# Kernel optimization log

Hardware: AMD Instinct MI355X
Metric: run time of the kernel (lower is better)

## Reference

```python
import jax, jax.numpy as jnp
import numpy as np

N, E, B = 10000, 160000, 256
IN, DESC = 57, 1217
# (in_dim, heads, out_per_head) for the 4 GATConv layers
CONV_DIMS = [(57, 5, 114), (570, 5, 171), (855, 5, 114), (570, 1, 570)]
FC_DIMS = [(1024 + DESC, 1024), (1024, 2048), (2048, 1024), (1024, 256), (256, 1)]


def setup_inputs() -> dict:
    key = jax.random.key(0)
    cnt = [0]
    def p(shape, scale=0.05):
        cnt[0] += 1
        return jax.random.normal(jax.random.fold_in(key, cnt[0]), shape, jnp.float32) * scale
    d = {}
    d["x"] = jax.random.normal(jax.random.fold_in(key, 100), (N, IN), jnp.float32)
    d["edge_index"] = jax.random.randint(jax.random.fold_in(key, 101), (2, E), 0, N)
    d["batch"] = jnp.sort(jax.random.randint(jax.random.fold_in(key, 102), (N,), 0, B))
    d["desc"] = jax.random.normal(jax.random.fold_in(key, 103), (B, DESC), jnp.float32)
    for i, (ci, H, C) in enumerate(CONV_DIMS, 1):
        d[f"W{i}"] = p((ci, H * C))
        d[f"as{i}"] = p((H, C))
        d[f"ad{i}"] = p((H, C))
        d[f"b{i}"] = jnp.zeros((H * C,), jnp.float32)
    d["Wg"] = p((570, 1024)); d["bg"] = jnp.zeros((1024,), jnp.float32)
    for i, (ci, co) in enumerate(FC_DIMS, 1):
        d[f"Wf{i}"] = p((ci, co))
        d[f"bf{i}"] = jnp.zeros((co,), jnp.float32)
    return d


def gat_conv(x, src, dst, W, a_src, a_dst, b):
    """PyG GATConv (eval mode: attention dropout off), self-loops already in src/dst."""
    n = x.shape[0]
    H, C = a_src.shape
    h = (x @ W).reshape(n, H, C)                      # [N,H,C]
    al_s = (h * a_src).sum(-1)                         # [N,H]
    al_d = (h * a_dst).sum(-1)                         # [N,H]
    e = jax.nn.leaky_relu(al_s[src] + al_d[dst], 0.2)  # [E,H]
    # segment softmax over destination node
    m = jax.ops.segment_max(e, dst, num_segments=n)
    e = jnp.exp(e - m[dst])
    s = jax.ops.segment_sum(e, dst, num_segments=n)
    alpha = e / (s[dst] + 1e-16)                       # [E,H]
    msg = h[src] * alpha[:, :, None]                   # [E,H,C]
    out = jax.ops.segment_sum(msg, dst, num_segments=n)
    return out.reshape(n, H * C) + b


def reference(x, edge_index, batch, desc,
              W1, as1, ad1, b1, W2, as2, ad2, b2,
              W3, as3, ad3, b3, W4, as4, ad4, b4,
              Wg, bg, Wf1, bf1, Wf2, bf2, Wf3, bf3, Wf4, bf4, Wf5, bf5):
    n = x.shape[0]
    loops = jnp.arange(n)
    src = jnp.concatenate([edge_index[0], loops])
    dst = jnp.concatenate([edge_index[1], loops])
    h = x
    for W, a_s, a_d, b in [(W1, as1, ad1, b1), (W2, as2, ad2, b2),
                           (W3, as3, ad3, b3), (W4, as4, ad4, b4)]:
        h = jax.nn.relu(gat_conv(h, src, dst, W, a_s, a_d, b))
    pooled = jax.ops.segment_sum(h, batch, num_segments=B)   # global_add_pool [B,570]
    g = pooled @ Wg + bg
    z = jnp.concatenate([g, desc], axis=1)                    # [B, 2241]
    z = jax.nn.relu(z @ Wf1 + bf1)
    z = jax.nn.relu(z @ Wf2 + bf2)
    z = jax.nn.relu(z @ Wf3 + bf3)
    z = jax.nn.relu(z @ Wf4 + bf4)
    return z @ Wf5 + bf5                                      # [B,1]
```

## Files before the change

kernel.cpp:

```cpp
#include <hip/hip_runtime.h>
#include <hip/hip_bf16.h>
#include <math.h>

#define NNODES 10000
#define NEDGES 160000
#define NB     256
#define ETOT   (NEDGES + NNODES)
#define INDIM  57
#define DESCD  1217

static inline size_t align256(size_t x) { return (x + 255) & ~size_t(255); }

typedef _Float16 half8_t __attribute__((ext_vector_type(8)));
typedef _Float16 half4v_t __attribute__((ext_vector_type(4)));
typedef _Float16 half2_t __attribute__((ext_vector_type(2)));
typedef float f32x4 __attribute__((ext_vector_type(4)));

__device__ inline float wave_max(float v) {
#pragma unroll
  for (int o = 32; o > 0; o >>= 1) v = fmaxf(v, __shfl_xor(v, o));
  return v;
}
__device__ inline float wave_sum(float v) {
#pragma unroll
  for (int o = 32; o > 0; o >>= 1) v += __shfl_xor(v, o);
  return v;
}

__global__ void count_kernel(const int* __restrict__ ei, int* __restrict__ deg) {
  int e = blockIdx.x * blockDim.x + threadIdx.x;
  if (e < ETOT) {
    int dst = (e < NEDGES) ? ei[NEDGES + e] : (e - NEDGES);
    atomicAdd(&deg[dst], 1);
  }
}

__global__ __launch_bounds__(1024) void scan_kernel(const int* __restrict__ deg,
                                                    int* __restrict__ row_ptr,
                                                    int* __restrict__ cursor) {
  __shared__ int part[1024];
  const int CHUNK = (NNODES + 1023) / 1024;
  int t = threadIdx.x;
  int start = t * CHUNK;
  int sum = 0;
  for (int i = 0; i < CHUNK; ++i) {
    int idx = start + i;
    if (idx < NNODES) sum += deg[idx];
  }
  part[t] = sum;
  __syncthreads();
  for (int off = 1; off < 1024; off <<= 1) {
    int v = (t >= off) ? part[t - off] : 0;
    __syncthreads();
    part[t] += v;
    __syncthreads();
  }
  int run = (t > 0) ? part[t - 1] : 0;
  for (int i = 0; i < CHUNK; ++i) {
    int idx = start + i;
    if (idx < NNODES) {
      row_ptr[idx] = run;
      cursor[idx] = run;
      run += deg[idx];
    }
  }
  if (t == 1023) row_ptr[NNODES] = ETOT;
}

__global__ void scatter_kernel(const int* __restrict__ ei, int* __restrict__ cursor,
                               int* __restrict__ csr_src) {
  int e = blockIdx.x * blockDim.x + threadIdx.x;
  if (e < ETOT) {
    int src, dst;
    if (e < NEDGES) { src = ei[e]; dst = ei[NEDGES + e]; }
    else            { src = e - NEDGES; dst = src; }
    int idx = atomicAdd(&cursor[dst], 1);
    csr_src[idx] = src;
  }
}

__global__ void convert_x_kernel(const float* __restrict__ x, _Float16* __restrict__ x16) {
  int t = blockIdx.x * blockDim.x + threadIdx.x;
  if (t >= NNODES * 64) return;
  int n = t >> 6, k = t & 63;
  x16[t] = (_Float16)((k < INDIM) ? x[n * INDIM + k] : 0.f);
}

struct TMat { const float* src; _Float16* dst; int K, N, Kpad, tiles_k, tile_base;
              int Cn, Cnp, Ck, Ckp; };
struct TParams { TMat m[9]; };

__global__ __launch_bounds__(256) void transpose_w_kernel(TParams P, int nm) {
  __shared__ float tile[64][65];
  int bt = blockIdx.x;
  int mi = 0;
#pragma unroll
  for (int i = 1; i < 9; ++i)
    if (i < nm && bt >= P.m[i].tile_base) mi = i;
  TMat m = P.m[mi];
  int lt = bt - m.tile_base;
  int tk = lt % m.tiles_k, tn = lt / m.tiles_k;
  int k0 = tk * 64, n0 = tn * 64;
  int c = threadIdx.x & 63, r4 = threadIdx.x >> 6;
#pragma unroll
  for (int i = 0; i < 16; ++i) {
    int kr = r4 + i * 4;
    int gk = k0 + kr, gn = n0 + c;
    tile[kr][c] = (gk < m.K && gn < m.N) ? m.src[(size_t)gk * m.N + gn] : 0.f;
  }
  __syncthreads();
#pragma unroll
  for (int i = 0; i < 16; ++i) {
    int nr = r4 + i * 4;
    int gn = n0 + nr, gk = k0 + c;
    if (gn < m.N && gk < m.K) {
      int np = gn + (gn / m.Cn) * (m.Cnp - m.Cn);
      int kp = gk + (gk / m.Ck) * (m.Ckp - m.Ck);
      m.dst[(size_t)np * m.Kpad + kp] = (_Float16)tile[c][nr];
    }
  }
}

struct LMat { const float* W; const float* as; const float* ad; _Float16* dst;
              int K, HC, C, H, Kpad, la, wave_base, Ck, Ckp; };

__global__ __launch_bounds__(256) void logitw_kernel(LMat m0, LMat m1, LMat m2, LMat m3,
                                                     int nwaves) {
  int gw = (blockIdx.x * 256 + threadIdx.x) >> 6;
  int lane = threadIdx.x & 63;
  if (gw >= nwaves) return;
  LMat m = m3;
  if (gw < m1.wave_base) m = m0;
  else if (gw < m2.wave_base) m = m1;
  else if (gw < m3.wave_base) m = m2;
  int li = gw - m.wave_base;
  int H2 = 2 * m.H;
  int k = li / H2, r = li - k * H2;
  int h = (r >= m.H) ? r - m.H : r;
  const float* a = (r >= m.H) ? m.ad : m.as;
  float s = 0.f;
  for (int c = lane; c < m.C; c += 64)
    s += m.W[(size_t)k * m.HC + h * m.C + c] * a[h * m.C + c];
  s = wave_sum(s);
  int kp = k + (k / m.Ck) * (m.Ckp - m.Ck);
  if (lane == 0) m.dst[(size_t)(m.la + r) * m.Kpad + kp] = (_Float16)s;
}

__global__ void pooled16_kernel(const float* __restrict__ pooled, _Float16* __restrict__ p16) {
  int t = blockIdx.x * blockDim.x + threadIdx.x;
  if (t >= NB * 576) return;
  int b = t / 576, c = t - b * 576;
  p16[t] = (_Float16)((c < 570) ? pooled[b * 570 + c] : 0.f);
}

__global__ void desc_fill_kernel(const float* __restrict__ desc, _Float16* __restrict__ z16) {
  int t = blockIdx.x * blockDim.x + threadIdx.x;
  if (t >= NB * 1280) return;
  int b = t / 1280, i = t - b * 1280;
  z16[(size_t)b * 2304 + 1024 + i] = (_Float16)((i < DESCD) ? desc[b * DESCD + i] : 0.f);
}

__global__ __launch_bounds__(256) void mfma_gemm_kernel(
    const _Float16* __restrict__ A, const _Float16* __restrict__ Bt,
    _Float16* __restrict__ C, int M, int Kpad, int Nreal, int ldc) {
  __shared__ __align__(16) char smem[32768];
  char* AsB = smem;
  char* BsB = smem + 16384;
  int tid = threadIdx.x;
  int lane = tid & 63, wid = tid >> 6;
  int l15 = lane & 15, g = lane >> 4;
  int wr = wid >> 1, wc = wid & 1;
  int m0 = blockIdx.y * 128, n0 = blockIdx.x * 128;
  f32x4 acc[4][4];
#pragma unroll
  for (int i = 0; i < 4; ++i)
#pragma unroll
    for (int j = 0; j < 4; ++j) acc[i][j] = (f32x4){0.f, 0.f, 0.f, 0.f};

  int KT = Kpad >> 6;
  half8_t pa[4], pb[4];
#pragma unroll
  for (int i = 0; i < 4; ++i) {
    int r = i * 32 + (tid >> 3);
    int cs = (tid & 7) ^ (r & 7);
    int ga = min(m0 + r, M - 1);
    pa[i] = *(const half8_t*)(A + (size_t)ga * Kpad + cs * 8);
    pb[i] = *(const half8_t*)(Bt + (size_t)(n0 + r) * Kpad + cs * 8);
  }
  for (int kt = 0; kt < KT; ++kt) {
    __syncthreads();
#pragma unroll
    for (int i = 0; i < 4; ++i) {
      *(half8_t*)(AsB + i * 4096 + tid * 16) = pa[i];
      *(half8_t*)(BsB + i * 4096 + tid * 16) = pb[i];
    }
    __syncthreads();
    if (kt + 1 < KT) {
      int k0 = (kt + 1) << 6;
#pragma unroll
      for (int i = 0; i < 4; ++i) {
        int r = i * 32 + (tid >> 3);
        int cs = (tid & 7) ^ (r & 7);
        int ga = min(m0 + r, M - 1);
        pa[i] = *(const half8_t*)(A + (size_t)ga * Kpad + k0 + cs * 8);
        pb[i] = *(const half8_t*)(Bt + (size_t)(n0 + r) * Kpad + k0 + cs * 8);
      }
    }
#pragma unroll
    for (int kk = 0; kk < 2; ++kk) {
      half8_t af[4], bf[4];
#pragma unroll
      for (int f = 0; f < 4; ++f) {
        int ra = wr * 64 + f * 16 + l15;
        af[f] = *(const half8_t*)(AsB + ra * 128 + (((kk * 4 + g) ^ (ra & 7)) << 4));
        int cb = wc * 64 + f * 16 + l15;
        bf[f] = *(const half8_t*)(BsB + cb * 128 + (((kk * 4 + g) ^ (cb & 7)) << 4));
      }
#pragma unroll
      for (int fm = 0; fm < 4; ++fm)
#pragma unroll
        for (int fn = 0; fn < 4; ++fn)
          acc[fm][fn] = __builtin_amdgcn_mfma_f32_16x16x32_f16(af[fm], bf[fn], acc[fm][fn], 0, 0, 0);
    }
  }
#pragma unroll
  for (int fm = 0; fm < 4; ++fm) {
    int gmb = m0 + wr * 64 + fm * 16 + g * 4;
#pragma unroll
    for (int fn = 0; fn < 4; ++fn) {
      int gn = n0 + wc * 64 + fn * 16 + l15;
      if (gn >= Nreal) continue;
#pragma unroll
      for (int j = 0; j < 4; ++j) {
        int gm = gmb + j;
        if (gm < M) C[(size_t)gm * ldc + gn] = (_Float16)acc[fm][fn][j];
      }
    }
  }
}

__global__ __launch_bounds__(256) void mfma_splitk_kernel(
    const _Float16* __restrict__ A, const _Float16* __restrict__ Bt,
    float* __restrict__ P, int M, int Kpad, int N, int ktpc) {
  __shared__ __align__(16) char smem[32768];
  char* AsB = smem;
  char* BsB = smem + 16384;
  int tid = threadIdx.x;
  int lane = tid & 63, wid = tid >> 6;
  int l15 = lane & 15, g = lane >> 4;
  int wr = wid >> 1, wc = wid & 1;
  int m0 = blockIdx.y * 128, n0 = blockIdx.x * 128;
  int z = blockIdx.z;
  int KT = Kpad >> 6;
  int ktb = z * ktpc;
  int kte = min(KT, ktb + ktpc);
  f32x4 acc[4][4];
#pragma unroll
  for (int i = 0; i < 4; ++i)
#pragma unroll
    for (int j = 0; j < 4; ++j) acc[i][j] = (f32x4){0.f, 0.f, 0.f, 0.f};

  half8_t pa[4], pb[4];
  {
    int k0 = ktb << 6;
#pragma unroll
    for (int i = 0; i < 4; ++i) {
      int r = i * 32 + (tid >> 3);
      int cs = (tid & 7) ^ (r & 7);
      int ga = min(m0 + r, M - 1);
      pa[i] = *(const half8_t*)(A + (size_t)ga * Kpad + k0 + cs * 8);
      pb[i] = *(const half8_t*)(Bt + (size_t)(n0 + r) * Kpad + k0 + cs * 8);
    }
  }
  for (int kt = ktb; kt < kte; ++kt) {
    __syncthreads();
#pragma unroll
    for (int i = 0; i < 4; ++i) {
      *(half8_t*)(AsB + i * 4096 + tid * 16) = pa[i];
      *(half8_t*)(BsB + i * 4096 + tid * 16) = pb[i];
    }
    __syncthreads();
    if (kt + 1 < kte) {
      int k0 = (kt + 1) << 6;
#pragma unroll
      for (int i = 0; i < 4; ++i) {
        int r = i * 32 + (tid >> 3);
        int cs = (tid & 7) ^ (r & 7);
        int ga = min(m0 + r, M - 1);
        pa[i] = *(const half8_t*)(A + (size_t)ga * Kpad + k0 + cs * 8);
        pb[i] = *(const half8_t*)(Bt + (size_t)(n0 + r) * Kpad + k0 + cs * 8);
      }
    }
#pragma unroll
    for (int kk = 0; kk < 2; ++kk) {
      half8_t af[4], bf[4];
#pragma unroll
      for (int f = 0; f < 4; ++f) {
        int ra = wr * 64 + f * 16 + l15;
        af[f] = *(const half8_t*)(AsB + ra * 128 + (((kk * 4 + g) ^ (ra & 7)) << 4));
        int cb = wc * 64 + f * 16 + l15;
        bf[f] = *(const half8_t*)(BsB + cb * 128 + (((kk * 4 + g) ^ (cb & 7)) << 4));
      }
#pragma unroll
      for (int fm = 0; fm < 4; ++fm)
#pragma unroll
        for (int fn = 0; fn < 4; ++fn)
          acc[fm][fn] = __builtin_amdgcn_mfma_f32_16x16x32_f16(af[fm], bf[fn], acc[fm][fn], 0, 0, 0);
    }
  }
  size_t zb = (size_t)z * M;
#pragma unroll
  for (int fm = 0; fm < 4; ++fm) {
    int gmb = m0 + wr * 64 + fm * 16 + g * 4;
#pragma unroll
    for (int fn = 0; fn < 4; ++fn) {
      int gn = n0 + wc * 64 + fn * 16 + l15;
      if (gn >= N) continue;
#pragma unroll
      for (int j = 0; j < 4; ++j) {
        int gm = gmb + j;
        if (gm < M) P[(zb + gm) * N + gn] = acc[fm][fn][j];
      }
    }
  }
}

__global__ void reduce16_kernel(const float* __restrict__ P, const float* __restrict__ bias,
                                _Float16* __restrict__ O, int M, int N, int ldo,
                                int S, int relu) {
  int idx = blockIdx.x * blockDim.x + threadIdx.x;
  if (idx >= M * ldo) return;
  int row = idx / ldo, col = idx - row * ldo;
  if (col >= N) return;
  float s = bias[col];
  int MN = M * N;
  for (int z = 0; z < S; ++z) s += P[(size_t)z * MN + row * N + col];
  if (relu) s = fmaxf(s, 0.f);
  O[idx] = (_Float16)s;
}

__global__ __launch_bounds__(256) void fc5_kernel(const _Float16* __restrict__ A,
                                                  const float* __restrict__ w,
                                                  const float* __restrict__ b,
                                                  float* __restrict__ out) {
  int wid = threadIdx.x >> 6, lane = threadIdx.x & 63;
  int m = blockIdx.x * 4 + wid;
  if (m >= NB) return;
  float s = 0.f;
  for (int k = lane; k < 256; k += 64) s += (float)A[m * 256 + k] * w[k];
  s = wave_sum(s);
  if (lane == 0) out[m] = s + b[0];
}

template <int H>
__global__ __launch_bounds__(256) void att_kernel_t(const _Float16* __restrict__ hbuf,
                                                    int ldh, int la,
                                                    const int* __restrict__ row_ptr,
                                                    const int* __restrict__ csr_src,
                                                    _Float16* __restrict__ alpha_t) {
  int wid = threadIdx.x >> 6, lane = threadIdx.x & 63;
  int n = blockIdx.x * 4 + wid;
  if (n >= NNODES) return;
  int rp = row_ptr[n], deg = row_ptr[n + 1] - rp;
  float ad[H], m[H], e0[H], e1[H], ssum[H];
#pragma unroll
  for (int h = 0; h < H; ++h) {
    ad[h] = (float)hbuf[(size_t)n * ldh + la + H + h];
    m[h] = -1e30f; ssum[h] = 0.f;
  }
  for (int j = lane, it = 0; j < deg; j += 64, ++it) {
    int s = csr_src[rp + j];
    half8_t v = *(const half8_t*)(hbuf + (size_t)s * ldh + la);
#pragma unroll
    for (int h = 0; h < H; ++h) {
      float e = (float)v[h] + ad[h];
      e = (e >= 0.f) ? e : 0.2f * e;
      if (it == 0) e0[h] = e; else if (it == 1) e1[h] = e;
      m[h] = fmaxf(m[h], e);
    }
  }
#pragma unroll
  for (int h = 0; h < H; ++h) m[h] = wave_max(m[h]);
  for (int j = lane, it = 0; j < deg; j += 64, ++it) {
    half8_t v{};
    if (it >= 2) v = *(const half8_t*)(hbuf + (size_t)csr_src[rp + j] * ldh + la);
#pragma unroll
    for (int h = 0; h < H; ++h) {
      float e;
      if (it == 0) e = e0[h];
      else if (it == 1) e = e1[h];
      else { e = (float)v[h] + ad[h]; e = (e >= 0.f) ? e : 0.2f * e; }
      ssum[h] += expf(e - m[h]);
    }
  }
#pragma unroll
  for (int h = 0; h < H; ++h) ssum[h] = 1.f / (wave_sum(ssum[h]) + 1e-16f);
  for (int j = lane, it = 0; j < deg; j += 64, ++it) {
    half8_t v{};
    if (it >= 2) v = *(const half8_t*)(hbuf + (size_t)csr_src[rp + j] * ldh + la);
#pragma unroll
    for (int h = 0; h < H; ++h) {
      float e;
      if (it == 0) e = e0[h];
      else if (it == 1) e = e1[h];
      else { e = (float)v[h] + ad[h]; e = (e >= 0.f) ? e : 0.2f * e; }
      alpha_t[(size_t)h * ETOT + rp + j] = (_Float16)(expf(e - m[h]) * ssum[h]);
    }
  }
}

__global__ __launch_bounds__(256) void agg_kernel(const _Float16* __restrict__ hbuf,
                                                  const _Float16* __restrict__ alpha_t,
                                                  const int* __restrict__ row_ptr,
                                                  const int* __restrict__ csr_src,
                                                  const float* __restrict__ bias,
                                                  _Float16* __restrict__ h16o,
                                                  int C, int Cpad, int ldh, int ldo,
                                                  int HCpad, int nchunks) {
  int wid = threadIdx.x >> 6, lane = threadIdx.x & 63;
  int gw = blockIdx.x * 4 + wid;
  int n = gw / nchunks, chunk = gw - n * nchunks;
  if (n >= NNODES) return;
  int k0 = chunk * 512 + lane * 8;
  if (k0 >= ldo) return;
  _Float16* op = h16o + (size_t)n * ldo + k0;
  if (k0 >= HCpad) { *(half8_t*)op = (half8_t){}; return; }
  int h0 = k0 / Cpad;
  int off = k0 - h0 * Cpad;
  const _Float16* A0 = alpha_t + (size_t)h0 * ETOT;
  const _Float16* hb = hbuf + k0;
  int rp = row_ptr[n], re = row_ptr[n + 1];
  half2_t acc0{}, acc1{}, acc2{}, acc3{};
  auto step = [&](int s, _Float16 a) {
    half8_t v = *(const half8_t*)(hb + (size_t)s * ldh);
    half2_t av{a, a};
    acc0 += av * half2_t{v[0], v[1]};
    acc1 += av * half2_t{v[2], v[3]};
    acc2 += av * half2_t{v[4], v[5]};
    acc3 += av * half2_t{v[6], v[7]};
  };
  int j = rp;
  for (; j < re && (j & 3); ++j) step(csr_src[j], A0[j]);
  for (; j + 8 <= re; j += 8) {
    int4 sa = *(const int4*)(csr_src + j);
    int4 sb = *(const int4*)(csr_src + j + 4);
    half4v_t aa = *(const half4v_t*)(A0 + j);
    half4v_t ab = *(const half4v_t*)(A0 + j + 4);
    step(sa.x, aa[0]); step(sa.y, aa[1]); step(sa.z, aa[2]); step(sa.w, aa[3]);
    step(sb.x, ab[0]); step(sb.y, ab[1]); step(sb.z, ab[2]); step(sb.w, ab[3]);
  }
  for (; j + 4 <= re; j += 4) {
    int4 sa = *(const int4*)(csr_src + j);
    half4v_t aa = *(const half4v_t*)(A0 + j);
    step(sa.x, aa[0]); step(sa.y, aa[1]); step(sa.z, aa[2]); step(sa.w, aa[3]);
  }
  for (; j < re; ++j) step(csr_src[j], A0[j]);
  int base = h0 * C + off;
  int nreal = C - off;
  float af[8] = {(float)acc0[0], (float)acc0[1], (float)acc1[0], (float)acc1[1],
                 (float)acc2[0], (float)acc2[1], (float)acc3[0], (float)acc3[1]};
  half8_t o;
#pragma unroll
  for (int i = 0; i < 8; ++i) {
    float bv = bias[base + ((i < nreal) ? i : 0)];
    o[i] = (i < nreal) ? (_Float16)fmaxf(af[i] + bv, 0.f) : (_Float16)0.f;
  }
  *(half8_t*)op = o;
}

__global__ __launch_bounds__(256) void pool_kernel(const _Float16* __restrict__ h4,
                                                   const int* __restrict__ batch,
                                                   float* __restrict__ pooled, int F, int ldh) {
  int wid = threadIdx.x >> 6, lane = threadIdx.x & 63;
  int n = blockIdx.x * 4 + wid;
  if (n >= NNODES) return;
  int b = batch[n];
  for (int k = lane; k < F; k += 64)
    atomicAdd(&pooled[(size_t)b * F + k], (float)h4[(size_t)n * ldh + k]);
}

extern "C" void kernel_launch(void* const* d_in, const int* in_sizes, int n_in,
                              void* d_out, int out_size, void* d_ws, size_t ws_size,
                              hipStream_t stream) {
  const float* x    = (const float*)d_in[0];
  const int*   ei   = (const int*)d_in[1];
  const int*   batch= (const int*)d_in[2];
  const float* desc = (const float*)d_in[3];
  const float* W1 = (const float*)d_in[4];  const float* as1 = (const float*)d_in[5];
  const float* ad1 = (const float*)d_in[6]; const float* b1 = (const float*)d_in[7];
  const float* W2 = (const float*)d_in[8];  const float* as2 = (const float*)d_in[9];
  const float* ad2 = (const float*)d_in[10];const float* b2 = (const float*)d_in[11];
  const float* W3 = (const float*)d_in[12]; const float* as3 = (const float*)d_in[13];
  const float* ad3 = (const float*)d_in[14];const float* b3 = (const float*)d_in[15];
  const float* W4 = (const float*)d_in[16]; const float* as4 = (const float*)d_in[17];
  const float* ad4 = (const float*)d_in[18];const float* b4 = (const float*)d_in[19];
  const float* Wg = (const float*)d_in[20]; const float* bg = (const float*)d_in[21];
  const float* Wf1 = (const float*)d_in[22];const float* bf1 = (const float*)d_in[23];
  const float* Wf2 = (const float*)d_in[24];const float* bf2 = (const float*)d_in[25];
  const float* Wf3 = (const float*)d_in[26];const float* bf3 = (const float*)d_in[27];
  const float* Wf4 = (const float*)d_in[28];const float* bf4 = (const float*)d_in[29];
  const float* Wf5 = (const float*)d_in[30];const float* bf5 = (const float*)d_in[31];
  float* out = (float*)d_out;

  char* p = (char*)d_ws;
  size_t off = 0;
  auto alloc = [&](size_t bytes) -> char* {
    char* r = p + off;
    off = align256(off + bytes);
    return r;
  };
  int*      deg     = (int*)alloc(sizeof(int) * NNODES);
  int*      row_ptr = (int*)alloc(sizeof(int) * (NNODES + 1));
  int*      cursor  = (int*)alloc(sizeof(int) * NNODES);
  int*      csr_src = (int*)alloc(sizeof(int) * ETOT);
  _Float16* alpha_t = (_Float16*)alloc(sizeof(_Float16) * (size_t)5 * ETOT);
  _Float16* x16     = (_Float16*)alloc(sizeof(_Float16) * (size_t)NNODES * 64);
  _Float16* hA16    = (_Float16*)alloc(sizeof(_Float16) * ((size_t)NNODES * 896 + 1024));
  _Float16* h16     = (_Float16*)alloc(sizeof(_Float16) * ((size_t)NNODES * 896 + 1024));
  size_t wt_begin = off;
  _Float16* WtL1 = (_Float16*)alloc(sizeof(_Float16) * 640 * 64);
  _Float16* WtL2 = (_Float16*)alloc(sizeof(_Float16) * 896 * 640);
  _Float16* WtL3 = (_Float16*)alloc(sizeof(_Float16) * 640 * 896);
  _Float16* WtL4 = (_Float16*)alloc(sizeof(_Float16) * 640 * 640);
  _Float16* WtG  = (_Float16*)alloc(sizeof(_Float16) * 1024 * 576);
  _Float16* WtF1 = (_Float16*)alloc(sizeof(_Float16) * 1024 * 2304);
  _Float16* WtF2 = (_Float16*)alloc(sizeof(_Float16) * 2048 * 1024);
  _Float16* WtF3 = (_Float16*)alloc(sizeof(_Float16) * 1024 * 2048);
  _Float16* WtF4 = (_Float16*)alloc(sizeof(_Float16) * 256 * 1024);
  size_t wt_end = off;
  float*    pooled  = (float*)alloc(sizeof(float) * NB * 570);
  _Float16* p16     = (_Float16*)alloc(sizeof(_Float16) * NB * 576);
  _Float16* z16     = (_Float16*)alloc(sizeof(_Float16) * NB * 2304);
  _Float16* t16     = (_Float16*)alloc(sizeof(_Float16) * NB * 2048);
  _Float16* u16     = (_Float16*)alloc(sizeof(_Float16) * NB * 2048);
  _Float16* v16     = (_Float16*)alloc(sizeof(_Float16) * NB * 256);
  (void)ws_size;

  hipMemsetAsync(deg, 0, sizeof(int) * NNODES, stream);
  {
    dim3 g((ETOT + 255) / 256);
    count_kernel<<<g, 256, 0, stream>>>(ei, deg);
    scan_kernel<<<1, 1024, 0, stream>>>(deg, row_ptr, cursor);
    scatter_kernel<<<g, 256, 0, stream>>>(ei, cursor, csr_src);
  }
  convert_x_kernel<<<(NNODES * 64 + 255) / 256, 256, 0, stream>>>(x, x16);

  hipMemsetAsync(p + wt_begin, 0, wt_end - wt_begin, stream);
  {
    auto tiles = [](int K, int N) { return ((K + 63) / 64) * ((N + 63) / 64); };
    TParams tp;
    int base = 0;
    auto add = [&](int i, const float* src, _Float16* dst, int K, int N, int Kpad,
                   int Cn, int Cnp, int Ck, int Ckp) {
      tp.m[i] = { src, dst, K, N, Kpad, (K + 63) / 64, base, Cn, Cnp, Ck, Ckp };
      base += tiles(K, N);
    };
    add(0, W1,  WtL1, INDIM,        570,   64, 114, 120, INDIM, INDIM);
    add(1, W2,  WtL2, 570,          855,  640, 171, 176, 114, 120);
    add(2, W3,  WtL3, 855,          570,  896, 114, 120, 171, 176);
    add(3, W4,  WtL4, 570,          570,  640, 570, 570, 114, 120);
    add(4, Wg,  WtG,  570,          1024,  576, 1024, 1024, 570, 570);
    add(5, Wf1, WtF1, 1024 + DESCD, 1024, 2304, 1024, 1024, 2304, 2304);
    add(6, Wf2, WtF2, 1024,         2048, 1024, 2048, 2048, 1024, 1024);
    add(7, Wf3, WtF3, 2048,         1024, 2048, 1024, 1024, 2048, 2048);
    add(8, Wf4, WtF4, 1024,          256, 1024, 256, 256, 1024, 1024);
    transpose_w_kernel<<<base, 256, 0, stream>>>(tp, 9);
  }
  {
    LMat m0 = { W1, as1, ad1, WtL1, INDIM, 570, 114, 5,  64, 600, 0, INDIM, INDIM };
    LMat m1 = { W2, as2, ad2, WtL2, 570,   855, 171, 5, 640, 880, INDIM * 10, 114, 120 };
    LMat m2 = { W3, as3, ad3, WtL3, 855,   570, 114, 5, 896, 600, INDIM * 10 + 5700, 171, 176 };
    LMat m3 = { W4, as4, ad4, WtL4, 570,   570, 570, 1, 640, 576, INDIM * 10 + 5700 + 8550, 114, 120 };
    int nwaves = INDIM * 10 + 5700 + 8550 + 1140;
    logitw_kernel<<<(nwaves * 64 + 255) / 256, 256, 0, stream>>>(m0, m1, m2, m3, nwaves);
  }

  dim3 gnode((NNODES + 3) / 4);

  struct LayerDef { _Float16* Wt; const float* b;
                    int H, C, Cpad, HCpad, Kpad, Npad, ldh, la, Nreal, ldo; };
  LayerDef L[4] = {
    { WtL1, b1, 5, 114, 120, 600,  64, 640, 616, 600, 610, 640 },
    { WtL2, b2, 5, 171, 176, 880, 640, 896, 896, 880, 890, 896 },
    { WtL3, b3, 5, 114, 120, 600, 896, 640, 616, 600, 610, 640 },
    { WtL4, b4, 1, 570, 576, 576, 640, 640, 584, 576, 578, 576 },
  };
  for (int l = 0; l < 4; ++l) {
    {
      const _Float16* Ain = (l == 0) ? x16 : h16;
      dim3 g(L[l].Npad / 128, (NNODES + 127) / 128);
      mfma_gemm_kernel<<<g, 256, 0, stream>>>(Ain, L[l].Wt, hA16, NNODES, L[l].Kpad,
                                              L[l].Nreal, L[l].ldh);
    }
    if (L[l].H == 5)
      att_kernel_t<5><<<gnode, 256, 0, stream>>>(hA16, L[l].ldh, L[l].la,
                                                 row_ptr, csr_src, alpha_t);
    else
      att_kernel_t<1><<<gnode, 256, 0, stream>>>(hA16, L[l].ldh, L[l].la,
                                                 row_ptr, csr_src, alpha_t);
    {
      int nchunks = (L[l].ldo + 511) / 512;
      dim3 g((NNODES * nchunks + 3) / 4);
      agg_kernel<<<g, 256, 0, stream>>>(hA16, alpha_t, row_ptr, csr_src, L[l].b, h16,
                                        L[l].C, L[l].Cpad, L[l].ldh, L[l].ldo,
                                        L[l].HCpad, nchunks);
    }
  }

  hipMemsetAsync(pooled, 0, sizeof(float) * NB * 570, stream);
  pool_kernel<<<gnode, 256, 0, stream>>>(h16, batch, pooled, 570, 576);

  float* partials = (float*)hA16;
  auto head_gemm = [&](const _Float16* A, const _Float16* Wt, const float* bias,
                       _Float16* O, int Kpad, int N, int ldo, int relu,
                       int ktpc, int S) {
    dim3 g(N / 128, NB / 128, S);
    mfma_splitk_kernel<<<g, 256, 0, stream>>>(A, Wt, partials, NB, Kpad, N, ktpc);
    int totO = NB * ldo;
    reduce16_kernel<<<(totO + 255) / 256, 256, 0, stream>>>(partials, bias, O, NB, N, ldo, S, relu);
  };

  pooled16_kernel<<<(NB * 576 + 255) / 256, 256, 0, stream>>>(pooled, p16);
  head_gemm(p16, WtG, bg, z16, 576, 1024, 2304, 0, 3, 3);
  desc_fill_kernel<<<(NB * 1280 + 255) / 256, 256, 0, stream>>>(desc, z16);
  head_gemm(z16, WtF1, bf1, t16, 2304, 1024, 1024, 1, 3, 12);
  head_gemm(t16, WtF2, bf2, u16, 1024, 2048, 2048, 1, 2, 8);
  head_gemm(u16, WtF3, bf3, t16, 2048, 1024, 1024, 1, 2, 16);
  head_gemm(t16, WtF4, bf4, v16, 1024,  256,  256, 1, 1, 16);
  fc5_kernel<<<(NB + 3) / 4, 256, 0, stream>>>(v16, Wf5, bf5, out);
}
```

Before: 462.2 us.

## Replace atomic pooling with sorted-batch segment reduction; remap agg waves chunk-major with XCD swizzle

Global add pooling now uses one block per graph. The block binary-searches the sorted batch array for its node range, sums the features directly and writes fp16. This removes the float atomics, the memset and the separate conversion kernel. The aggregation kernel now orders waves chunk-major (chunk outer, node inner) and swizzles block IDs across 8 groups, presumably to improve cache locality per XCD. The pooling rewrite relies on batch being sorted, which the task guarantees, and gives only 256 blocks with serial per-column loops.

```diff
diff --git a/kernel.cpp b/kernel.cpp
--- a/kernel.cpp
+++ b/kernel.cpp
@@ -146,13 +146,6 @@
   if (lane == 0) m.dst[(size_t)(m.la + r) * m.Kpad + kp] = (_Float16)s;
 }
 
-__global__ void pooled16_kernel(const float* __restrict__ pooled, _Float16* __restrict__ p16) {
-  int t = blockIdx.x * blockDim.x + threadIdx.x;
-  if (t >= NB * 576) return;
-  int b = t / 576, c = t - b * 576;
-  p16[t] = (_Float16)((c < 570) ? pooled[b * 570 + c] : 0.f);
-}
-
 __global__ void desc_fill_kernel(const float* __restrict__ desc, _Float16* __restrict__ z16) {
   int t = blockIdx.x * blockDim.x + threadIdx.x;
   if (t >= NB * 1280) return;
@@ -418,9 +411,13 @@
                                                   int C, int Cpad, int ldh, int ldo,
                                                   int HCpad, int nchunks) {
   int wid = threadIdx.x >> 6, lane = threadIdx.x & 63;
-  int gw = blockIdx.x * 4 + wid;
-  int n = gw / nchunks, chunk = gw - n * nchunks;
-  if (n >= NNODES) return;
+  int nb8 = gridDim.x >> 3;
+  int bid = blockIdx.x;
+  int swz = (bid & 7) * nb8 + (bid >> 3);
+  int gw = swz * 4 + wid;
+  int chunk = gw / NNODES;
+  int n = gw - chunk * NNODES;
+  if (chunk >= nchunks) return;
   int k0 = chunk * 512 + lane * 8;
   if (k0 >= ldo) return;
   _Float16* op = h16o + (size_t)n * ldo + k0;
@@ -470,13 +467,23 @@
 
 __global__ __launch_bounds__(256) void pool_kernel(const _Float16* __restrict__ h4,
                                                    const int* __restrict__ batch,
-                                                   float* __restrict__ pooled, int F, int ldh) {
-  int wid = threadIdx.x >> 6, lane = threadIdx.x & 63;
-  int n = blockIdx.x * 4 + wid;
-  if (n >= NNODES) return;
-  int b = batch[n];
-  for (int k = lane; k < F; k += 64)
-    atomicAdd(&pooled[(size_t)b * F + k], (float)h4[(size_t)n * ldh + k]);
+                                                   _Float16* __restrict__ p16) {
+  int b = blockIdx.x;
+  __shared__ int se[2];
+  if (threadIdx.x < 2) {
+    int target = b + threadIdx.x;
+    int lo = 0, hi = NNODES;
+    while (lo < hi) { int mid = (lo + hi) >> 1; if (batch[mid] < target) lo = mid + 1; else hi = mid; }
+    se[threadIdx.x] = lo;
+  }
+  __syncthreads();
+  int s = se[0], e = se[1];
+  for (int c = threadIdx.x; c < 576; c += 256) {
+    float acc = 0.f;
+    if (c < 570)
+      for (int n = s; n < e; ++n) acc += (float)h4[(size_t)n * 576 + c];
+    p16[b * 576 + c] = (_Float16)acc;
+  }
 }
 
 extern "C" void kernel_launch(void* const* d_in, const int* in_sizes, int n_in,
@@ -528,7 +535,6 @@
   _Float16* WtF3 = (_Float16*)alloc(sizeof(_Float16) * 1024 * 2048);
   _Float16* WtF4 = (_Float16*)alloc(sizeof(_Float16) * 256 * 1024);
   size_t wt_end = off;
-  float*    pooled  = (float*)alloc(sizeof(float) * NB * 570);
   _Float16* p16     = (_Float16*)alloc(sizeof(_Float16) * NB * 576);
   _Float16* z16     = (_Float16*)alloc(sizeof(_Float16) * NB * 2304);
   _Float16* t16     = (_Float16*)alloc(sizeof(_Float16) * NB * 2048);
@@ -600,15 +606,16 @@
                                                  row_ptr, csr_src, alpha_t);
     {
       int nchunks = (L[l].ldo + 511) / 512;
-      dim3 g((NNODES * nchunks + 3) / 4);
-      agg_kernel<<<g, 256, 0, stream>>>(hA16, alpha_t, row_ptr, csr_src, L[l].b, h16,
-                                        L[l].C, L[l].Cpad, L[l].ldh, L[l].ldo,
-                                        L[l].HCpad, nchunks);
-    }
-  }
-
-  hipMemsetAsync(pooled, 0, sizeof(float) * NB * 570, stream);
-  pool_kernel<<<gnode, 256, 0, stream>>>(h16, batch, pooled, 570, 576);
+      int nwaves = nchunks * NNODES;
+      int nblocks = (nwaves + 3) / 4;
+      nblocks = ((nblocks + 7) / 8) * 8;
+      agg_kernel<<<nblocks, 256, 0, stream>>>(hA16, alpha_t, row_ptr, csr_src, L[l].b, h16,
+                                              L[l].C, L[l].Cpad, L[l].ldh, L[l].ldo,
+                                              L[l].HCpad, nchunks);
+    }
+  }
+
+  pool_kernel<<<NB, 256, 0, stream>>>(h16, batch, p16);
 
   float* partials = (float*)hA16;
   auto head_gemm = [&](const _Float16* A, const _Float16* Wt, const float* bias,
@@ -620,7 +627,6 @@
     reduce16_kernel<<<(totO + 255) / 256, 256, 0, stream>>>(partials, bias, O, NB, N, ldo, S, relu);
   };
 
-  pooled16_kernel<<<(NB * 576 + 255) / 256, 256, 0, stream>>>(pooled, p16);
   head_gemm(p16, WtG, bg, z16, 576, 1024, 2304, 0, 3, 3);
   desc_fill_kernel<<<(NB * 1280 + 255) / 256, 256, 0, stream>>>(desc, z16);
   head_gemm(z16, WtF1, bf1, t16, 2304, 1024, 1024, 1, 3, 12);
```

Result: slower. 503.8 us (+9.0%).

## Cache leaky-relu scores and defer softmax normalization to aggregation

Applied to the files above, without the earlier changes.

The attention kernel stores per-edge leaky-relu logits in an fp16 buffer during the max pass instead of re-gathering source rows. It then merges the sum and alpha-writing passes into one, writing unnormalized exponentials, and stores the per-node inverse sum separately. The aggregation kernel applies that inverse sum once per output. This removes one pass and repeated random gathers, at the cost of an extra edge-sized buffer and fp16 rounding of logits and unnormalized weights.

```diff
diff --git a/kernel.cpp b/kernel.cpp
--- a/kernel.cpp
+++ b/kernel.cpp
@@ -357,55 +357,49 @@
                                                     int ldh, int la,
                                                     const int* __restrict__ row_ptr,
                                                     const int* __restrict__ csr_src,
-                                                    _Float16* __restrict__ alpha_t) {
+                                                    _Float16* __restrict__ alpha_t,
+                                                    half8_t* __restrict__ e8,
+                                                    float* __restrict__ sinv) {
   int wid = threadIdx.x >> 6, lane = threadIdx.x & 63;
   int n = blockIdx.x * 4 + wid;
   if (n >= NNODES) return;
   int rp = row_ptr[n], deg = row_ptr[n + 1] - rp;
-  float ad[H], m[H], e0[H], e1[H], ssum[H];
+  float ad[H], m[H], ssum[H];
 #pragma unroll
   for (int h = 0; h < H; ++h) {
     ad[h] = (float)hbuf[(size_t)n * ldh + la + H + h];
     m[h] = -1e30f; ssum[h] = 0.f;
   }
-  for (int j = lane, it = 0; j < deg; j += 64, ++it) {
+  for (int j = lane; j < deg; j += 64) {
     int s = csr_src[rp + j];
     half8_t v = *(const half8_t*)(hbuf + (size_t)s * ldh + la);
+    half8_t ev{};
 #pragma unroll
     for (int h = 0; h < H; ++h) {
       float e = (float)v[h] + ad[h];
       e = (e >= 0.f) ? e : 0.2f * e;
-      if (it == 0) e0[h] = e; else if (it == 1) e1[h] = e;
+      ev[h] = (_Float16)e;
       m[h] = fmaxf(m[h], e);
     }
-  }
-#pragma unroll
-  for (int h = 0; h < H; ++h) m[h] = wave_max(m[h]);
-  for (int j = lane, it = 0; j < deg; j += 64, ++it) {
-    half8_t v{};
-    if (it >= 2) v = *(const half8_t*)(hbuf + (size_t)csr_src[rp + j] * ldh + la);
+    e8[rp + j] = ev;
+  }
+#pragma unroll
+  for (int h = 0; h < H; ++h) m[h] = wave_max(fmaxf(m[h], -1e30f));
+  for (int j = lane; j < deg; j += 64) {
+    half8_t ev = e8[rp + j];
 #pragma unroll
     for (int h = 0; h < H; ++h) {
-      float e;
-      if (it == 0) e = e0[h];
-      else if (it == 1) e = e1[h];
-      else { e = (float)v[h] + ad[h]; e = (e >= 0.f) ? e : 0.2f * e; }
-      ssum[h] += expf(e - m[h]);
-    }
-  }
-#pragma unroll
-  for (int h = 0; h < H; ++h) ssum[h] = 1.f / (wave_sum(ssum[h]) + 1e-16f);
-  for (int j = lane, it = 0; j < deg; j += 64, ++it) {
-    half8_t v{};
-    if (it >= 2) v = *(const half8_t*)(hbuf + (size_t)csr_src[rp + j] * ldh + la);
-#pragma unroll
-    for (int h = 0; h < H; ++h) {
-      float e;
-      if (it == 0) e = e0[h];
-      else if (it == 1) e = e1[h];
-      else { e = (float)v[h] + ad[h]; e = (e >= 0.f) ? e : 0.2f * e; }
-      alpha_t[(size_t)h * ETOT + rp + j] = (_Float16)(expf(e - m[h]) * ssum[h]);
-    }
+      float e = (float)ev[h] - m[h];
+      e = (e > 0.f) ? 0.f : e;
+      float x = expf(e);
+      ssum[h] += x;
+      alpha_t[(size_t)h * ETOT + rp + j] = (_Float16)x;
+    }
+  }
+#pragma unroll
+  for (int h = 0; h < H; ++h) {
+    float s = wave_sum(ssum[h]);
+    if (lane == 0) sinv[h * NNODES + n] = 1.f / (s + 1e-16f);
   }
 }
 
@@ -414,6 +408,7 @@
                                                   const int* __restrict__ row_ptr,
                                                   const int* __restrict__ csr_src,
                                                   const float* __restrict__ bias,
+                                                  const float* __restrict__ sinv,
                                                   _Float16* __restrict__ h16o,
                                                   int C, int Cpad, int ldh, int ldo,
                                                   int HCpad, int nchunks) {
@@ -455,6 +450,7 @@
     step(sa.x, aa[0]); step(sa.y, aa[1]); step(sa.z, aa[2]); step(sa.w, aa[3]);
   }
   for (; j < re; ++j) step(csr_src[j], A0[j]);
+  float sc = sinv[h0 * NNODES + n];
   int base = h0 * C + off;
   int nreal = C - off;
   float af[8] = {(float)acc0[0], (float)acc0[1], (float)acc1[0], (float)acc1[1],
@@ -463,7 +459,7 @@
 #pragma unroll
   for (int i = 0; i < 8; ++i) {
     float bv = bias[base + ((i < nreal) ? i : 0)];
-    o[i] = (i < nreal) ? (_Float16)fmaxf(af[i] + bv, 0.f) : (_Float16)0.f;
+    o[i] = (i < nreal) ? (_Float16)fmaxf(af[i] * sc + bv, 0.f) : (_Float16)0.f;
   }
   *(half8_t*)op = o;
 }
@@ -514,6 +510,8 @@
   int*      cursor  = (int*)alloc(sizeof(int) * NNODES);
   int*      csr_src = (int*)alloc(sizeof(int) * ETOT);
   _Float16* alpha_t = (_Float16*)alloc(sizeof(_Float16) * (size_t)5 * ETOT);
+  half8_t*  e8      = (half8_t*)alloc(sizeof(half8_t) * (size_t)ETOT);
+  float*    sinv    = (float*)alloc(sizeof(float) * 5 * NNODES);
   _Float16* x16     = (_Float16*)alloc(sizeof(_Float16) * (size_t)NNODES * 64);
   _Float16* hA16    = (_Float16*)alloc(sizeof(_Float16) * ((size_t)NNODES * 896 + 1024));
   _Float16* h16     = (_Float16*)alloc(sizeof(_Float16) * ((size_t)NNODES * 896 + 1024));
@@ -594,14 +592,14 @@
     }
     if (L[l].H == 5)
       att_kernel_t<5><<<gnode, 256, 0, stream>>>(hA16, L[l].ldh, L[l].la,
-                                                 row_ptr, csr_src, alpha_t);
+                                                 row_ptr, csr_src, alpha_t, e8, sinv);
     else
       att_kernel_t<1><<<gnode, 256, 0, stream>>>(hA16, L[l].ldh, L[l].la,
-                                                 row_ptr, csr_src, alpha_t);
+                                                 row_ptr, csr_src, alpha_t, e8, sinv);
     {
       int nchunks = (L[l].ldo + 511) / 512;
       dim3 g((NNODES * nchunks + 3) / 4);
-      agg_kernel<<<g, 256, 0, stream>>>(hA16, alpha_t, row_ptr, csr_src, L[l].b, h16,
+      agg_kernel<<<g, 256, 0, stream>>>(hA16, alpha_t, row_ptr, csr_src, L[l].b, sinv, h16,
                                         L[l].C, L[l].Cpad, L[l].ldh, L[l].ldo,
                                         L[l].HCpad, nchunks);
     }
```

Result: no change. 467.2 us (+1.1%).
